# Performance work log

Measured on AMD Instinct MI355X. Metric: run time of the kernel, lower is better.

The kernel has to match this reference:

```python
import jax, jax.numpy as jnp
import numpy as np

NW, WS, VALID, D, H, DFF = 1024, 128, 112, 256, 8, 1024
DH = D // H
N = NW * VALID


def setup_inputs() -> dict:
    key = jax.random.key(0)
    ks = jax.random.split(key, 12)
    src = jax.random.normal(ks[0], (N, D), dtype=jnp.float32)
    pos = jax.random.normal(ks[1], (NW, WS, D), dtype=jnp.float32)
    tok = jnp.arange(N, dtype=jnp.int32)
    flat_inds = (tok // VALID) * WS + (tok % VALID)  # slot in padded [NW*WS] layout
    key_padding_mask = jnp.broadcast_to(jnp.arange(WS) >= VALID, (NW, WS))  # True = pad
    s = 0.02
    return {
        "src": src,
        "pos": pos,
        "flat_inds": flat_inds,
        "key_padding_mask": key_padding_mask,
        "in_proj_w": jax.random.normal(ks[2], (3 * D, D), dtype=jnp.float32) * s,
        "in_proj_b": jnp.zeros((3 * D,), jnp.float32),
        "out_proj_w": jax.random.normal(ks[3], (D, D), dtype=jnp.float32) * s,
        "out_proj_b": jnp.zeros((D,), jnp.float32),
        "w1": jax.random.normal(ks[4], (DFF, D), dtype=jnp.float32) * s,
        "b1": jnp.zeros((DFF,), jnp.float32),
        "w2": jax.random.normal(ks[5], (D, DFF), dtype=jnp.float32) * s,
        "b2": jnp.zeros((D,), jnp.float32),
        "ln1_g": jnp.ones((D,), jnp.float32),
        "ln1_b": jnp.zeros((D,), jnp.float32),
        "ln2_g": jnp.ones((D,), jnp.float32),
        "ln2_b": jnp.zeros((D,), jnp.float32),
    }


def _layer_norm(x, g, b, eps=1e-5):
    mu = jnp.mean(x, axis=-1, keepdims=True)
    var = jnp.mean(jnp.square(x - mu), axis=-1, keepdims=True)
    return (x - mu) * jax.lax.rsqrt(var + eps) * g + b


def reference(src, pos, flat_inds, key_padding_mask, in_proj_w, in_proj_b,
              out_proj_w, out_proj_b, w1, b1, w2, b2, ln1_g, ln1_b, ln2_g, ln2_b):
    # flat2window_v2: scatter flat tokens into padded [NW, WS, D] windows
    x3 = jnp.zeros((NW * WS, D), src.dtype).at[flat_inds].set(src).reshape(NW, WS, D)
    qk_in = x3 + pos  # pos added to q and k only, not v
    q = qk_in @ in_proj_w[:D].T + in_proj_b[:D]
    k = qk_in @ in_proj_w[D:2 * D].T + in_proj_b[D:2 * D]
    v = x3 @ in_proj_w[2 * D:].T + in_proj_b[2 * D:]
    q = q.reshape(NW, WS, H, DH)
    k = k.reshape(NW, WS, H, DH)
    v = v.reshape(NW, WS, H, DH)
    scores = jnp.einsum('nqhd,nkhd->nhqk', q, k) / np.sqrt(DH).astype(np.float32)
    neg = jnp.finfo(scores.dtype).min
    scores = jnp.where(key_padding_mask[:, None, None, :], neg, scores)
    attn = jax.nn.softmax(scores, axis=-1)
    o = jnp.einsum('nhqk,nkhd->nqhd', attn, v).reshape(NW, WS, D)
    o = o @ out_proj_w.T + out_proj_b
    # window2flat_v2: gather back to flat layout
    attn_out = o.reshape(NW * WS, D)[flat_inds]
    h = _layer_norm(src + attn_out, ln1_g, ln1_b)
    ffn = jax.nn.relu(h @ w1.T + b1) @ w2.T + b2
    out = _layer_norm(h + ffn, ln2_g, ln2_b)
    return out
```

## Files before the change

### kernel.cpp

```cpp
#include <hip/hip_runtime.h>
#include <stdint.h>

#define NWIN   1024
#define WSZ    128
#define NVAL   112
#define DMODEL 256
#define NHEAD  8
#define DHEAD  32
#define DFFN   1024
#define NTOK   (NWIN * NVAL)

typedef short bf16x8 __attribute__((ext_vector_type(8)));
typedef float f32x4  __attribute__((ext_vector_type(4)));

__device__ __forceinline__ unsigned short f2b(float f) {
  union { float f; uint32_t u; } x; x.f = f;
  uint32_t r = x.u + 0x7fffu + ((x.u >> 16) & 1u);
  return (unsigned short)(r >> 16);
}
__device__ __forceinline__ uint32_t f2b2(float lo, float hi) {
  return (uint32_t)f2b(lo) | ((uint32_t)f2b(hi) << 16);
}
__device__ __forceinline__ float b2f(unsigned short u) {
  union { uint32_t u; float f; } x; x.u = (uint32_t)u << 16; return x.f;
}
__device__ __forceinline__ void gload_lds16(const void* g, void* l) {
  __builtin_amdgcn_global_load_lds((const __attribute__((address_space(1))) unsigned int*)g,
                                   (__attribute__((address_space(3))) unsigned int*)l, 16, 0, 0);
}

__global__ __launch_bounds__(256)
void cvt_all(const float* __restrict__ w0, const float* __restrict__ w1,
             const float* __restrict__ w2, const float* __restrict__ w3,
             unsigned short* __restrict__ out) {
  int i = blockIdx.x * 256 + threadIdx.x;
  if (i >= 196608) return;
  const float* src; int local;
  if (i < 49152)        { src = w0; local = i; }
  else if (i < 65536)   { src = w1; local = i - 49152; }
  else if (i < 131072)  { src = w2; local = i - 65536; }
  else                  { src = w3; local = i - 131072; }
  float4 v = ((const float4*)src)[local];
  ((uint2*)out)[i] = make_uint2(f2b2(v.x, v.y), f2b2(v.z, v.w));
}

__global__ __launch_bounds__(256)
void prep_x(const float* __restrict__ src, const float* __restrict__ pos,
            unsigned short* __restrict__ xb, unsigned short* __restrict__ qkb) {
  int i = blockIdx.x * 256 + threadIdx.x;
  const int total = NTOK * 64;
  int stride = gridDim.x * 256;
  for (; i < total; i += stride) {
    int n = i >> 6, c = i & 63;
    int w = n / NVAL;
    int s = n - w * NVAL;
    float4 sv = ((const float4*)src)[i];
    float4 pv = ((const float4*)pos)[(size_t)(w * WSZ + s) * 64 + c];
    ((uint2*)xb)[i]  = make_uint2(f2b2(sv.x, sv.y), f2b2(sv.z, sv.w));
    ((uint2*)qkb)[i] = make_uint2(f2b2(sv.x + pv.x, sv.y + pv.y),
                                  f2b2(sv.z + pv.z, sv.w + pv.w));
  }
}

template<int K, int EPI>
__global__ __launch_bounds__(256)
void gemm_bf16(const unsigned short* __restrict__ A, const unsigned short* __restrict__ A2,
               int colSplit, const unsigned short* __restrict__ B,
               const float* __restrict__ bias,
               unsigned short* __restrict__ outb, int NX, int NY, int ldo) {
  __shared__ unsigned short As[128 * 64];
  __shared__ unsigned short Bs[128 * 64];

  int bid = blockIdx.x;
  int xcd = bid & 7;
  int idx = bid >> 3;
  int bx = idx % NX;
  int by = xcd * (NY >> 3) + idx / NX;
  int m0 = by * 128, n0 = bx * 128;
  const unsigned short* Ap = (n0 >= colSplit) ? A2 : A;

  int t = threadIdx.x;
  int wid = t >> 6, lane = t & 63;
  int wr = wid >> 1, wc = wid & 1;
  int lr = lane & 15, lk = lane >> 4;

  f32x4 acc[4][4];
#pragma unroll
  for (int i = 0; i < 4; i++)
#pragma unroll
    for (int j = 0; j < 4; j++) acc[i][j] = (f32x4){0.f, 0.f, 0.f, 0.f};

  for (int kt = 0; kt < K / 64; ++kt) {
    int k0 = kt * 64;
#pragma unroll
    for (int i = 0; i < 4; ++i) {
      int p = wid * 4096 + i * 1024 + lane * 16;
      int row = p >> 7;
      int kbs = (p & 127) ^ ((row & 7) << 4);
      gload_lds16(Ap + (size_t)(m0 + row) * K + k0 + (kbs >> 1),
                  (char*)As + wid * 4096 + i * 1024);
      gload_lds16(B + (size_t)(n0 + row) * K + k0 + (kbs >> 1),
                  (char*)Bs + wid * 4096 + i * 1024);
    }
    __syncthreads();
#pragma unroll
    for (int ks = 0; ks < 2; ++ks) {
      bf16x8 af[4], bfr[4];
#pragma unroll
      for (int mi = 0; mi < 4; mi++) {
        int R = wr * 64 + mi * 16 + lr;
        int q = R * 128 + ks * 64 + lk * 16;
        af[mi] = *(const bf16x8*)((const char*)As + (q ^ ((R & 7) << 4)));
      }
#pragma unroll
      for (int ni = 0; ni < 4; ni++) {
        int R = wc * 64 + ni * 16 + lr;
        int q = R * 128 + ks * 64 + lk * 16;
        bfr[ni] = *(const bf16x8*)((const char*)Bs + (q ^ ((R & 7) << 4)));
      }
#pragma unroll
      for (int mi = 0; mi < 4; mi++)
#pragma unroll
        for (int ni = 0; ni < 4; ni++)
          acc[mi][ni] = __builtin_amdgcn_mfma_f32_16x16x32_bf16(af[mi], bfr[ni], acc[mi][ni], 0, 0, 0);
    }
    __syncthreads();
  }

#pragma unroll
  for (int ni = 0; ni < 4; ++ni) {
    int n = n0 + wc * 64 + ni * 16 + lr;
    float bv = bias[n];
#pragma unroll
    for (int mi = 0; mi < 4; ++mi) {
      int mbase = m0 + wr * 64 + mi * 16 + 4 * lk;
#pragma unroll
      for (int r = 0; r < 4; ++r) {
        int m = mbase + r;
        float v = acc[mi][ni][r] + bv;
        if (EPI == 1) v = v > 0.f ? v : 0.f;
        outb[(size_t)m * ldo + n] = f2b(v);
      }
    }
  }
}

__global__ __launch_bounds__(256)
void attn_kernel(const unsigned short* __restrict__ qkv, unsigned short* __restrict__ attnb) {
  __shared__ unsigned short Qs[128 * 40];
  __shared__ unsigned short Ks[128 * 40];
  __shared__ unsigned short Vt[32 * 136];
  __shared__ unsigned short Ps[128 * 136];

  int w = blockIdx.x >> 3, h = blockIdx.x & 7;
  int t = threadIdx.x;
  int lane = t & 63, wid = t >> 6;

  {
    int r = t >> 1, hf = t & 1;
    uint4 z = make_uint4(0, 0, 0, 0);
    uint4 a0 = z, a1 = z, b0 = z, b1 = z, c0 = z, c1 = z;
    if (r < NVAL) {
      size_t base = ((size_t)(w * NVAL + r)) * 768 + h * 32 + hf * 16;
      const uint4* q4 = (const uint4*)(qkv + base);       a0 = q4[0]; a1 = q4[1];
      const uint4* k4 = (const uint4*)(qkv + base + 256); b0 = k4[0]; b1 = k4[1];
      const uint4* v4 = (const uint4*)(qkv + base + 512); c0 = v4[0]; c1 = v4[1];
    }
    uint4* qs4 = (uint4*)(Qs + r * 40 + hf * 16); qs4[0] = a0; qs4[1] = a1;
    uint4* ks4 = (uint4*)(Ks + r * 40 + hf * 16); ks4[0] = b0; ks4[1] = b1;
    union { uint4 v[2]; unsigned short u[16]; } tmp;
    tmp.v[0] = c0; tmp.v[1] = c1;
#pragma unroll
    for (int j = 0; j < 16; j++) Vt[(hf * 16 + j) * 136 + r] = tmp.u[j];
  }
  __syncthreads();

  int lr = lane & 15, lk = lane >> 4;
  int m0 = wid * 32;

  f32x4 sc[2][8];
#pragma unroll
  for (int i = 0; i < 2; i++)
#pragma unroll
    for (int j = 0; j < 8; j++) sc[i][j] = (f32x4){0.f, 0.f, 0.f, 0.f};
  bf16x8 qa[2];
#pragma unroll
  for (int mi = 0; mi < 2; mi++)
    qa[mi] = *(const bf16x8*)(Qs + (m0 + mi * 16 + lr) * 40 + lk * 8);
#pragma unroll
  for (int ni = 0; ni < 8; ni++) {
    bf16x8 kb = *(const bf16x8*)(Ks + (ni * 16 + lr) * 40 + lk * 8);
#pragma unroll
    for (int mi = 0; mi < 2; mi++)
      sc[mi][ni] = __builtin_amdgcn_mfma_f32_16x16x32_bf16(qa[mi], kb, sc[mi][ni], 0, 0, 0);
  }

  const float scale = 0.1767766952966369f;
#pragma unroll
  for (int mi = 0; mi < 2; mi++) {
#pragma unroll
    for (int r = 0; r < 4; r++) {
      float mx = -1e30f;
#pragma unroll
      for (int ni = 0; ni < 8; ni++) {
        float v = sc[mi][ni][r] * scale;
        if (ni * 16 + lr >= NVAL) v = -1e30f;
        sc[mi][ni][r] = v;
        mx = fmaxf(mx, v);
      }
#pragma unroll
      for (int off = 1; off < 16; off <<= 1) mx = fmaxf(mx, __shfl_xor(mx, off));
      float sum = 0.f;
#pragma unroll
      for (int ni = 0; ni < 8; ni++) {
        float p = __expf(sc[mi][ni][r] - mx);
        sc[mi][ni][r] = p;
        sum += p;
      }
#pragma unroll
      for (int off = 1; off < 16; off <<= 1) sum += __shfl_xor(sum, off);
      float inv = 1.f / sum;
      int row = m0 + mi * 16 + 4 * lk + r;
#pragma unroll
      for (int ni = 0; ni < 8; ni++)
        Ps[row * 136 + ni * 16 + lr] = f2b(sc[mi][ni][r] * inv);
    }
  }
  __syncthreads();

  f32x4 oc[2][2];
#pragma unroll
  for (int i = 0; i < 2; i++)
#pragma unroll
    for (int j = 0; j < 2; j++) oc[i][j] = (f32x4){0.f, 0.f, 0.f, 0.f};
#pragma unroll
  for (int ks = 0; ks < 4; ks++) {
    bf16x8 pa[2];
#pragma unroll
    for (int mi = 0; mi < 2; mi++)
      pa[mi] = *(const bf16x8*)(Ps + (m0 + mi * 16 + lr) * 136 + ks * 32 + lk * 8);
#pragma unroll
    for (int ni = 0; ni < 2; ni++) {
      bf16x8 vb = *(const bf16x8*)(Vt + (ni * 16 + lr) * 136 + ks * 32 + lk * 8);
#pragma unroll
      for (int mi = 0; mi < 2; mi++)
        oc[mi][ni] = __builtin_amdgcn_mfma_f32_16x16x32_bf16(pa[mi], vb, oc[mi][ni], 0, 0, 0);
    }
  }
#pragma unroll
  for (int mi = 0; mi < 2; mi++)
#pragma unroll
    for (int ni = 0; ni < 2; ni++)
#pragma unroll
      for (int r = 0; r < 4; r++) {
        int s = m0 + mi * 16 + 4 * lk + r;
        if (s < NVAL)
          attnb[((size_t)(w * NVAL + s)) * 256 + h * 32 + ni * 16 + lr] = f2b(oc[mi][ni][r]);
      }
}

__global__ __launch_bounds__(256)
void ln1_kernel(const float* __restrict__ src, const unsigned short* __restrict__ o1,
                const float* __restrict__ g, const float* __restrict__ b,
                unsigned short* __restrict__ h1b) {
  int wid = threadIdx.x >> 6, lane = threadIdx.x & 63;
  size_t row = (size_t)blockIdx.x * 4 + wid;
  float4 s4 = ((const float4*)src)[row * 64 + lane];
  uint2 o2 = ((const uint2*)o1)[row * 64 + lane];
  float4 x;
  x.x = s4.x + b2f((unsigned short)(o2.x & 0xffff));
  x.y = s4.y + b2f((unsigned short)(o2.x >> 16));
  x.z = s4.z + b2f((unsigned short)(o2.y & 0xffff));
  x.w = s4.w + b2f((unsigned short)(o2.y >> 16));
  float s = x.x + x.y + x.z + x.w;
  float q = x.x * x.x + x.y * x.y + x.z * x.z + x.w * x.w;
#pragma unroll
  for (int off = 1; off < 64; off <<= 1) { s += __shfl_xor(s, off); q += __shfl_xor(q, off); }
  float mean = s * (1.f / 256.f);
  float var = q * (1.f / 256.f) - mean * mean;
  float rstd = rsqrtf(var + 1e-5f);
  float4 gv = ((const float4*)g)[lane];
  float4 bv = ((const float4*)b)[lane];
  float4 y;
  y.x = (x.x - mean) * rstd * gv.x + bv.x;
  y.y = (x.y - mean) * rstd * gv.y + bv.y;
  y.z = (x.z - mean) * rstd * gv.z + bv.z;
  y.w = (x.w - mean) * rstd * gv.w + bv.w;
  ((uint2*)h1b)[row * 64 + lane] = make_uint2(f2b2(y.x, y.y), f2b2(y.z, y.w));
}

__global__ __launch_bounds__(256)
void ln2_kernel(const float* __restrict__ src, const unsigned short* __restrict__ o1,
                const unsigned short* __restrict__ f2,
                const float* __restrict__ g1, const float* __restrict__ b1,
                const float* __restrict__ g2, const float* __restrict__ b2,
                float* __restrict__ out) {
  int wid = threadIdx.x >> 6, lane = threadIdx.x & 63;
  size_t row = (size_t)blockIdx.x * 4 + wid;
  float4 s4 = ((const float4*)src)[row * 64 + lane];
  uint2 o2 = ((const uint2*)o1)[row * 64 + lane];
  float4 x;
  x.x = s4.x + b2f((unsigned short)(o2.x & 0xffff));
  x.y = s4.y + b2f((unsigned short)(o2.x >> 16));
  x.z = s4.z + b2f((unsigned short)(o2.y & 0xffff));
  x.w = s4.w + b2f((unsigned short)(o2.y >> 16));
  float s = x.x + x.y + x.z + x.w;
  float q = x.x * x.x + x.y * x.y + x.z * x.z + x.w * x.w;
#pragma unroll
  for (int off = 1; off < 64; off <<= 1) { s += __shfl_xor(s, off); q += __shfl_xor(q, off); }
  float mean = s * (1.f / 256.f);
  float var = q * (1.f / 256.f) - mean * mean;
  float rstd = rsqrtf(var + 1e-5f);
  float4 g1v = ((const float4*)g1)[lane];
  float4 b1v = ((const float4*)b1)[lane];
  uint2 fv = ((const uint2*)f2)[row * 64 + lane];
  float4 x2;
  x2.x = (x.x - mean) * rstd * g1v.x + b1v.x + b2f((unsigned short)(fv.x & 0xffff));
  x2.y = (x.y - mean) * rstd * g1v.y + b1v.y + b2f((unsigned short)(fv.x >> 16));
  x2.z = (x.z - mean) * rstd * g1v.z + b1v.z + b2f((unsigned short)(fv.y & 0xffff));
  x2.w = (x.w - mean) * rstd * g1v.w + b1v.w + b2f((unsigned short)(fv.y >> 16));
  float s2 = x2.x + x2.y + x2.z + x2.w;
  float q2 = x2.x * x2.x + x2.y * x2.y + x2.z * x2.z + x2.w * x2.w;
#pragma unroll
  for (int off = 1; off < 64; off <<= 1) { s2 += __shfl_xor(s2, off); q2 += __shfl_xor(q2, off); }
  float mean2 = s2 * (1.f / 256.f);
  float var2 = q2 * (1.f / 256.f) - mean2 * mean2;
  float rstd2 = rsqrtf(var2 + 1e-5f);
  float4 g2v = ((const float4*)g2)[lane];
  float4 b2v = ((const float4*)b2)[lane];
  float4 y;
  y.x = (x2.x - mean2) * rstd2 * g2v.x + b2v.x;
  y.y = (x2.y - mean2) * rstd2 * g2v.y + b2v.y;
  y.z = (x2.z - mean2) * rstd2 * g2v.z + b2v.z;
  y.w = (x2.w - mean2) * rstd2 * g2v.w + b2v.w;
  ((float4*)out)[row * 64 + lane] = y;
}

extern "C" void kernel_launch(void* const* d_in, const int* in_sizes, int n_in,
                              void* d_out, int out_size, void* d_ws, size_t ws_size,
                              hipStream_t stream) {
  const float* src = (const float*)d_in[0];
  const float* pos = (const float*)d_in[1];
  const float* ipw = (const float*)d_in[4];
  const float* ipb = (const float*)d_in[5];
  const float* opw = (const float*)d_in[6];
  const float* opb = (const float*)d_in[7];
  const float* w1  = (const float*)d_in[8];
  const float* b1  = (const float*)d_in[9];
  const float* w2  = (const float*)d_in[10];
  const float* b2  = (const float*)d_in[11];
  const float* g1  = (const float*)d_in[12];
  const float* be1 = (const float*)d_in[13];
  const float* g2  = (const float*)d_in[14];
  const float* be2 = (const float*)d_in[15];

  char* ws = (char*)d_ws;
  unsigned short* wbi  = (unsigned short*)(ws + 0);
  unsigned short* wbo  = (unsigned short*)(ws + 393216);
  unsigned short* wb1  = (unsigned short*)(ws + 524288);
  unsigned short* wb2  = (unsigned short*)(ws + 1048576);
  unsigned short* xb   = (unsigned short*)(ws + 1572864);
  unsigned short* qkb  = (unsigned short*)(ws + 60293120);
  unsigned short* qkvc = (unsigned short*)(ws + 119013376);
  unsigned short* attnb= (unsigned short*)(ws + 163053568);
  unsigned short* o1   = xb;
  unsigned short* h1b  = qkb;
  unsigned short* f1c  = qkvc;
  unsigned short* f2   = attnb;

  cvt_all<<<768, 256, 0, stream>>>(ipw, opw, w1, w2, wbi);
  prep_x<<<2048, 256, 0, stream>>>(src, pos, xb, qkb);

  const int MCQ = NTOK / 4;
  const int NYQ = MCQ / 128;
  for (int c = 0; c < 4; ++c) {
    size_t ro = (size_t)c * MCQ * 256;
    gemm_bf16<256, 0><<<6 * NYQ, 256, 0, stream>>>(qkb + ro, xb + ro, 512, wbi, ipb,
                                                   qkvc, 6, NYQ, 768);
    attn_kernel<<<(NWIN / 4) * NHEAD, 256, 0, stream>>>(qkvc, attnb + ro);
  }

  gemm_bf16<256, 0><<<2 * (NTOK / 128), 256, 0, stream>>>(attnb, nullptr, 1 << 30, wbo, opb,
                                                          o1, 2, NTOK / 128, 256);
  ln1_kernel<<<NTOK / 4, 256, 0, stream>>>(src, o1, g1, be1, h1b);

  const int MCF = NTOK / 8;
  const int NYF = MCF / 128;
  for (int c = 0; c < 8; ++c) {
    size_t ro = (size_t)c * MCF;
    gemm_bf16<256, 1><<<8 * NYF, 256, 0, stream>>>(h1b + ro * 256, nullptr, 1 << 30, wb1, b1,
                                                   f1c, 8, NYF, 1024);
    gemm_bf16<1024, 0><<<2 * NYF, 256, 0, stream>>>(f1c, nullptr, 1 << 30, wb2, b2,
                                                    f2 + ro * 256, 2, NYF, 256);
  }

  ln2_kernel<<<NTOK / 4, 256, 0, stream>>>(src, o1, f2, g1, be1, g2, be2, (float*)d_out);
}
```

Before: 0.9998 ms.

## Batch row processing, write FFN output as fp32 into output, halve chunk counts

```diff
diff --git a/kernel.cpp b/kernel.cpp
--- a/kernel.cpp
+++ b/kernel.cpp
@@ -47,18 +47,23 @@
 __global__ __launch_bounds__(256)
 void prep_x(const float* __restrict__ src, const float* __restrict__ pos,
             unsigned short* __restrict__ xb, unsigned short* __restrict__ qkb) {
-  int i = blockIdx.x * 256 + threadIdx.x;
-  const int total = NTOK * 64;
-  int stride = gridDim.x * 256;
-  for (; i < total; i += stride) {
-    int n = i >> 6, c = i & 63;
-    int w = n / NVAL;
-    int s = n - w * NVAL;
-    float4 sv = ((const float4*)src)[i];
-    float4 pv = ((const float4*)pos)[(size_t)(w * WSZ + s) * 64 + c];
-    ((uint2*)xb)[i]  = make_uint2(f2b2(sv.x, sv.y), f2b2(sv.z, sv.w));
-    ((uint2*)qkb)[i] = make_uint2(f2b2(sv.x + pv.x, sv.y + pv.y),
-                                  f2b2(sv.z + pv.z, sv.w + pv.w));
+  int wid = threadIdx.x >> 6, lane = threadIdx.x & 63;
+  int wv = blockIdx.x * 4 + wid;
+  const int NWAVE = gridDim.x * 4;
+  for (int row = wv; row < NTOK; row += 2 * NWAVE) {
+    int rowB = row + NWAVE;
+    int wA = row / NVAL,  sA = row - wA * NVAL;
+    int wB = rowB / NVAL, sB = rowB - wB * NVAL;
+    float4 sa = ((const float4*)src)[(size_t)row * 64 + lane];
+    float4 pa = ((const float4*)pos)[((size_t)(wA * WSZ + sA)) * 64 + lane];
+    float4 sb = ((const float4*)src)[(size_t)rowB * 64 + lane];
+    float4 pb = ((const float4*)pos)[((size_t)(wB * WSZ + sB)) * 64 + lane];
+    ((uint2*)xb)[(size_t)row * 64 + lane]   = make_uint2(f2b2(sa.x, sa.y), f2b2(sa.z, sa.w));
+    ((uint2*)qkb)[(size_t)row * 64 + lane]  = make_uint2(f2b2(sa.x + pa.x, sa.y + pa.y),
+                                                         f2b2(sa.z + pa.z, sa.w + pa.w));
+    ((uint2*)xb)[(size_t)rowB * 64 + lane]  = make_uint2(f2b2(sb.x, sb.y), f2b2(sb.z, sb.w));
+    ((uint2*)qkb)[(size_t)rowB * 64 + lane] = make_uint2(f2b2(sb.x + pb.x, sb.y + pb.y),
+                                                         f2b2(sb.z + pb.z, sb.w + pb.w));
   }
 }
 
@@ -67,7 +72,7 @@
 void gemm_bf16(const unsigned short* __restrict__ A, const unsigned short* __restrict__ A2,
                int colSplit, const unsigned short* __restrict__ B,
                const float* __restrict__ bias,
-               unsigned short* __restrict__ outb, int NX, int NY, int ldo) {
+               void* __restrict__ outp, int NX, int NY, int ldo) {
   __shared__ unsigned short As[128 * 64];
   __shared__ unsigned short Bs[128 * 64];
 
@@ -127,6 +132,8 @@
     __syncthreads();
   }
 
+  unsigned short* outb = (unsigned short*)outp;
+  float* outf = (float*)outp;
 #pragma unroll
   for (int ni = 0; ni < 4; ++ni) {
     int n = n0 + wc * 64 + ni * 16 + lr;
@@ -138,8 +145,10 @@
       for (int r = 0; r < 4; ++r) {
         int m = mbase + r;
         float v = acc[mi][ni][r] + bv;
-        if (EPI == 1) v = v > 0.f ? v : 0.f;
-        outb[(size_t)m * ldo + n] = f2b(v);
+        size_t o = (size_t)m * ldo + n;
+        if (EPI == 0) outb[o] = f2b(v);
+        else if (EPI == 1) outb[o] = f2b(v > 0.f ? v : 0.f);
+        else outf[o] = v;
       }
     }
   }
@@ -264,76 +273,84 @@
                 const float* __restrict__ g, const float* __restrict__ b,
                 unsigned short* __restrict__ h1b) {
   int wid = threadIdx.x >> 6, lane = threadIdx.x & 63;
-  size_t row = (size_t)blockIdx.x * 4 + wid;
-  float4 s4 = ((const float4*)src)[row * 64 + lane];
-  uint2 o2 = ((const uint2*)o1)[row * 64 + lane];
-  float4 x;
-  x.x = s4.x + b2f((unsigned short)(o2.x & 0xffff));
-  x.y = s4.y + b2f((unsigned short)(o2.x >> 16));
-  x.z = s4.z + b2f((unsigned short)(o2.y & 0xffff));
-  x.w = s4.w + b2f((unsigned short)(o2.y >> 16));
-  float s = x.x + x.y + x.z + x.w;
-  float q = x.x * x.x + x.y * x.y + x.z * x.z + x.w * x.w;
-#pragma unroll
-  for (int off = 1; off < 64; off <<= 1) { s += __shfl_xor(s, off); q += __shfl_xor(q, off); }
-  float mean = s * (1.f / 256.f);
-  float var = q * (1.f / 256.f) - mean * mean;
-  float rstd = rsqrtf(var + 1e-5f);
+  int wv = blockIdx.x * 4 + wid;
+  const int NWAVE = gridDim.x * 4;
   float4 gv = ((const float4*)g)[lane];
   float4 bv = ((const float4*)b)[lane];
-  float4 y;
-  y.x = (x.x - mean) * rstd * gv.x + bv.x;
-  y.y = (x.y - mean) * rstd * gv.y + bv.y;
-  y.z = (x.z - mean) * rstd * gv.z + bv.z;
-  y.w = (x.w - mean) * rstd * gv.w + bv.w;
-  ((uint2*)h1b)[row * 64 + lane] = make_uint2(f2b2(y.x, y.y), f2b2(y.z, y.w));
+  for (int row = wv; row < NTOK; row += 2 * NWAVE) {
+    int rowB = row + NWAVE;
+    float4 sa = ((const float4*)src)[(size_t)row * 64 + lane];
+    uint2  oa = ((const uint2*)o1)[(size_t)row * 64 + lane];
+    float4 sb = ((const float4*)src)[(size_t)rowB * 64 + lane];
+    uint2  ob = ((const uint2*)o1)[(size_t)rowB * 64 + lane];
+    float4 xA, xB;
+    xA.x = sa.x + b2f((unsigned short)(oa.x & 0xffff));
+    xA.y = sa.y + b2f((unsigned short)(oa.x >> 16));
+    xA.z = sa.z + b2f((unsigned short)(oa.y & 0xffff));
+    xA.w = sa.w + b2f((unsigned short)(oa.y >> 16));
+    xB.x = sb.x + b2f((unsigned short)(ob.x & 0xffff));
+    xB.y = sb.y + b2f((unsigned short)(ob.x >> 16));
+    xB.z = sb.z + b2f((unsigned short)(ob.y & 0xffff));
+    xB.w = sb.w + b2f((unsigned short)(ob.y >> 16));
+    float s1 = xA.x + xA.y + xA.z + xA.w, q1 = xA.x*xA.x + xA.y*xA.y + xA.z*xA.z + xA.w*xA.w;
+    float s2 = xB.x + xB.y + xB.z + xB.w, q2 = xB.x*xB.x + xB.y*xB.y + xB.z*xB.z + xB.w*xB.w;
+#pragma unroll
+    for (int off = 1; off < 64; off <<= 1) {
+      s1 += __shfl_xor(s1, off); q1 += __shfl_xor(q1, off);
+      s2 += __shfl_xor(s2, off); q2 += __shfl_xor(q2, off);
+    }
+    float m1 = s1 * (1.f/256.f), v1 = q1 * (1.f/256.f) - m1*m1, r1 = rsqrtf(v1 + 1e-5f);
+    float m2 = s2 * (1.f/256.f), v2 = q2 * (1.f/256.f) - m2*m2, r2 = rsqrtf(v2 + 1e-5f);
+    ((uint2*)h1b)[(size_t)row * 64 + lane] = make_uint2(
+        f2b2((xA.x - m1) * r1 * gv.x + bv.x, (xA.y - m1) * r1 * gv.y + bv.y),
+        f2b2((xA.z - m1) * r1 * gv.z + bv.z, (xA.w - m1) * r1 * gv.w + bv.w));
+    ((uint2*)h1b)[(size_t)rowB * 64 + lane] = make_uint2(
+        f2b2((xB.x - m2) * r2 * gv.x + bv.x, (xB.y - m2) * r2 * gv.y + bv.y),
+        f2b2((xB.z - m2) * r2 * gv.z + bv.z, (xB.w - m2) * r2 * gv.w + bv.w));
+  }
 }
 
 __global__ __launch_bounds__(256)
 void ln2_kernel(const float* __restrict__ src, const unsigned short* __restrict__ o1,
-                const unsigned short* __restrict__ f2,
                 const float* __restrict__ g1, const float* __restrict__ b1,
                 const float* __restrict__ g2, const float* __restrict__ b2,
-                float* __restrict__ out) {
+                float* __restrict__ io) {
   int wid = threadIdx.x >> 6, lane = threadIdx.x & 63;
-  size_t row = (size_t)blockIdx.x * 4 + wid;
-  float4 s4 = ((const float4*)src)[row * 64 + lane];
-  uint2 o2 = ((const uint2*)o1)[row * 64 + lane];
-  float4 x;
-  x.x = s4.x + b2f((unsigned short)(o2.x & 0xffff));
-  x.y = s4.y + b2f((unsigned short)(o2.x >> 16));
-  x.z = s4.z + b2f((unsigned short)(o2.y & 0xffff));
-  x.w = s4.w + b2f((unsigned short)(o2.y >> 16));
-  float s = x.x + x.y + x.z + x.w;
-  float q = x.x * x.x + x.y * x.y + x.z * x.z + x.w * x.w;
-#pragma unroll
-  for (int off = 1; off < 64; off <<= 1) { s += __shfl_xor(s, off); q += __shfl_xor(q, off); }
-  float mean = s * (1.f / 256.f);
-  float var = q * (1.f / 256.f) - mean * mean;
-  float rstd = rsqrtf(var + 1e-5f);
+  int wv = blockIdx.x * 4 + wid;
+  const int NWAVE = gridDim.x * 4;
   float4 g1v = ((const float4*)g1)[lane];
   float4 b1v = ((const float4*)b1)[lane];
-  uint2 fv = ((const uint2*)f2)[row * 64 + lane];
-  float4 x2;
-  x2.x = (x.x - mean) * rstd * g1v.x + b1v.x + b2f((unsigned short)(fv.x & 0xffff));
-  x2.y = (x.y - mean) * rstd * g1v.y + b1v.y + b2f((unsigned short)(fv.x >> 16));
-  x2.z = (x.z - mean) * rstd * g1v.z + b1v.z + b2f((unsigned short)(fv.y & 0xffff));
-  x2.w = (x.w - mean) * rstd * g1v.w + b1v.w + b2f((unsigned short)(fv.y >> 16));
-  float s2 = x2.x + x2.y + x2.z + x2.w;
-  float q2 = x2.x * x2.x + x2.y * x2.y + x2.z * x2.z + x2.w * x2.w;
-#pragma unroll
-  for (int off = 1; off < 64; off <<= 1) { s2 += __shfl_xor(s2, off); q2 += __shfl_xor(q2, off); }
-  float mean2 = s2 * (1.f / 256.f);
-  float var2 = q2 * (1.f / 256.f) - mean2 * mean2;
-  float rstd2 = rsqrtf(var2 + 1e-5f);
   float4 g2v = ((const float4*)g2)[lane];
   float4 b2v = ((const float4*)b2)[lane];
-  float4 y;
-  y.x = (x2.x - mean2) * rstd2 * g2v.x + b2v.x;
-  y.y = (x2.y - mean2) * rstd2 * g2v.y + b2v.y;
-  y.z = (x2.z - mean2) * rstd2 * g2v.z + b2v.z;
-  y.w = (x2.w - mean2) * rstd2 * g2v.w + b2v.w;
-  ((float4*)out)[row * 64 + lane] = y;
+  for (int row = wv; row < NTOK; row += NWAVE) {
+    float4 s4 = ((const float4*)src)[(size_t)row * 64 + lane];
+    uint2  o2 = ((const uint2*)o1)[(size_t)row * 64 + lane];
+    float4 fv = ((const float4*)io)[(size_t)row * 64 + lane];
+    float4 x;
+    x.x = s4.x + b2f((unsigned short)(o2.x & 0xffff));
+    x.y = s4.y + b2f((unsigned short)(o2.x >> 16));
+    x.z = s4.z + b2f((unsigned short)(o2.y & 0xffff));
+    x.w = s4.w + b2f((unsigned short)(o2.y >> 16));
+    float s = x.x + x.y + x.z + x.w, q = x.x*x.x + x.y*x.y + x.z*x.z + x.w*x.w;
+#pragma unroll
+    for (int off = 1; off < 64; off <<= 1) { s += __shfl_xor(s, off); q += __shfl_xor(q, off); }
+    float mean = s * (1.f/256.f), var = q * (1.f/256.f) - mean*mean, rstd = rsqrtf(var + 1e-5f);
+    float4 x2;
+    x2.x = (x.x - mean) * rstd * g1v.x + b1v.x + fv.x;
+    x2.y = (x.y - mean) * rstd * g1v.y + b1v.y + fv.y;
+    x2.z = (x.z - mean) * rstd * g1v.z + b1v.z + fv.z;
+    x2.w = (x.w - mean) * rstd * g1v.w + b1v.w + fv.w;
+    float s2 = x2.x + x2.y + x2.z + x2.w, q2 = x2.x*x2.x + x2.y*x2.y + x2.z*x2.z + x2.w*x2.w;
+#pragma unroll
+    for (int off = 1; off < 64; off <<= 1) { s2 += __shfl_xor(s2, off); q2 += __shfl_xor(q2, off); }
+    float mean2 = s2 * (1.f/256.f), var2 = q2 * (1.f/256.f) - mean2*mean2, rstd2 = rsqrtf(var2 + 1e-5f);
+    float4 y;
+    y.x = (x2.x - mean2) * rstd2 * g2v.x + b2v.x;
+    y.y = (x2.y - mean2) * rstd2 * g2v.y + b2v.y;
+    y.z = (x2.z - mean2) * rstd2 * g2v.z + b2v.z;
+    y.w = (x2.w - mean2) * rstd2 * g2v.w + b2v.w;
+    ((float4*)io)[(size_t)row * 64 + lane] = y;
+  }
 }
 
 extern "C" void kernel_launch(void* const* d_in, const int* in_sizes, int n_in,
@@ -362,37 +379,36 @@
   unsigned short* xb   = (unsigned short*)(ws + 1572864);
   unsigned short* qkb  = (unsigned short*)(ws + 60293120);
   unsigned short* qkvc = (unsigned short*)(ws + 119013376);
-  unsigned short* attnb= (unsigned short*)(ws + 163053568);
   unsigned short* o1   = xb;
+  unsigned short* attnb= qkb;
   unsigned short* h1b  = qkb;
   unsigned short* f1c  = qkvc;
-  unsigned short* f2   = attnb;
 
   cvt_all<<<768, 256, 0, stream>>>(ipw, opw, w1, w2, wbi);
   prep_x<<<2048, 256, 0, stream>>>(src, pos, xb, qkb);
 
-  const int MCQ = NTOK / 4;
+  const int MCQ = NTOK / 2;
   const int NYQ = MCQ / 128;
-  for (int c = 0; c < 4; ++c) {
+  for (int c = 0; c < 2; ++c) {
     size_t ro = (size_t)c * MCQ * 256;
     gemm_bf16<256, 0><<<6 * NYQ, 256, 0, stream>>>(qkb + ro, xb + ro, 512, wbi, ipb,
                                                    qkvc, 6, NYQ, 768);
-    attn_kernel<<<(NWIN / 4) * NHEAD, 256, 0, stream>>>(qkvc, attnb + ro);
+    attn_kernel<<<(NWIN / 2) * NHEAD, 256, 0, stream>>>(qkvc, attnb + ro);
   }
 
   gemm_bf16<256, 0><<<2 * (NTOK / 128), 256, 0, stream>>>(attnb, nullptr, 1 << 30, wbo, opb,
                                                           o1, 2, NTOK / 128, 256);
-  ln1_kernel<<<NTOK / 4, 256, 0, stream>>>(src, o1, g1, be1, h1b);
-
-  const int MCF = NTOK / 8;
+  ln1_kernel<<<1024, 256, 0, stream>>>(src, o1, g1, be1, h1b);
+
+  const int MCF = NTOK / 4;
   const int NYF = MCF / 128;
-  for (int c = 0; c < 8; ++c) {
+  for (int c = 0; c < 4; ++c) {
     size_t ro = (size_t)c * MCF;
     gemm_bf16<256, 1><<<8 * NYF, 256, 0, stream>>>(h1b + ro * 256, nullptr, 1 << 30, wb1, b1,
                                                    f1c, 8, NYF, 1024);
-    gemm_bf16<1024, 0><<<2 * NYF, 256, 0, stream>>>(f1c, nullptr, 1 << 30, wb2, b2,
-                                                    f2 + ro * 256, 2, NYF, 256);
-  }
-
-  ln2_kernel<<<NTOK / 4, 256, 0, stream>>>(src, o1, f2, g1, be1, g2, be2, (float*)d_out);
-}
+    gemm_bf16<1024, 2><<<2 * NYF, 256, 0, stream>>>(f1c, nullptr, 1 << 30, wb2, b2,
+                                                    (float*)d_out + ro * 256, 2, NYF, 256);
+  }
+
+  ln2_kernel<<<1024, 256, 0, stream>>>(src, o1, g1, be1, g2, be2, (float*)d_out);
+}
```

Measured after the change: 906.4 us. -9.3%, faster.
